# Kernel tuning notes

Hardware: AMD Instinct MI355X
Metric: run time of the kernel (lower is better)

The kernel has to match this reference:

```python
import jax, jax.numpy as jnp
import numpy as np

B, T, C, H = 16, 2048, 1024, 64

def setup_inputs() -> dict:
    key = jax.random.key(0)
    kx, kq, kk, kv = jax.random.split(key, 4)
    x = jax.random.normal(kx, (B, T, C), dtype=jnp.float32)
    Wq = jax.random.normal(kq, (C, H), dtype=jnp.float32) * (C ** -0.5)
    Wk = jax.random.normal(kk, (C, H), dtype=jnp.float32) * (C ** -0.5)
    Wv = jax.random.normal(kv, (C, H), dtype=jnp.float32) * (C ** -0.5)
    return {"x": x, "Wq": Wq, "Wk": Wk, "Wv": Wv}

def reference(x, Wq, Wk, Wv):
    # single causal self-attention head; dropout p=0.0 (identity)
    Tlen = x.shape[1]
    q = jnp.einsum('btc,ch->bth', x, Wq)  # [B,T,H]
    k = jnp.einsum('btc,ch->bth', x, Wk)
    v = jnp.einsum('btc,ch->bth', x, Wv)
    scale = q.shape[-1] ** -0.5
    scores = jnp.einsum('bth,bsh->bts', q, k) * scale  # [B,T,T]
    causal = jnp.tril(jnp.ones((Tlen, Tlen), dtype=bool))
    scores = jnp.where(causal, scores, -jnp.inf)
    weights = jax.nn.softmax(scores, axis=-1)
    out = jnp.einsum('bts,bsh->bth', weights, v)  # [B,T,H]
    return out
```

## Files before the change

### kernel.cpp

```cpp
#include <hip/hip_runtime.h>


typedef float  floatx4 __attribute__((ext_vector_type(4)));
typedef __bf16 bf16x8  __attribute__((ext_vector_type(8)));
typedef unsigned short ushort4v __attribute__((ext_vector_type(4)));
typedef unsigned int   uint2v   __attribute__((ext_vector_type(2)));
typedef unsigned int   uint4v   __attribute__((ext_vector_type(4)));

constexpr int Bn = 16;
constexpr int Tn = 2048;
constexpr int Cn = 1024;
constexpr int Hn = 64;
constexpr int BT = Bn * Tn;

constexpr float QSCALE = 0.125f * 1.44269504088896340736f;

__device__ __forceinline__ unsigned short f2b(float f) {
  unsigned int u = __builtin_bit_cast(unsigned int, f);
  u += 0x7fffu + ((u >> 16) & 1u);
  return (unsigned short)(u >> 16);
}

__device__ __forceinline__ unsigned int cvt_pk_bf16(float lo, float hi) {
  unsigned int r;
  asm("v_cvt_pk_bf16_f32 %0, %1, %2" : "=v"(r) : "v"(lo), "v"(hi));
  return r;
}

__global__ __launch_bounds__(256) void pack_w(const float* __restrict__ Wq,
                                              const float* __restrict__ Wk,
                                              const float* __restrict__ Wv,
                                              unsigned short* __restrict__ Wp) {
  int gid = blockIdx.x * 256 + threadIdx.x;
  int mat = gid >> 16;
  int rem = gid & 65535;
  int k   = rem >> 6;
  int col = rem & 63;
  const float* W = (mat == 0) ? Wq : (mat == 1) ? Wk : Wv;
  float v = W[rem];
  int kb = k >> 3, j = k & 7, ct = (mat << 2) | (col >> 4), c = col & 15;
  size_t idx = ((((size_t)ct * 128) + kb) * 16 + c) * 8 + j;
  Wp[idx] = f2b(v);
}

__global__ __launch_bounds__(256, 2) void proj_kernel(
    const float* __restrict__ x, const unsigned short* __restrict__ Wp,
    unsigned short* __restrict__ Q, unsigned short* __restrict__ K,
    unsigned short* __restrict__ Vt) {
  __shared__ alignas(16) unsigned short Bl[2][12 * 1024];

  const int tid  = threadIdx.x;
  const int wave = tid >> 6;
  const int lane = tid & 63;
  const int quad = lane >> 4;
  const int l16  = lane & 15;
  const int wr   = wave >> 1;
  const int wc   = wave & 1;
  const int rbase = blockIdx.x * 64;

  floatx4 acc[2][6];
#pragma unroll
  for (int a = 0; a < 2; ++a)
#pragma unroll
    for (int b = 0; b < 6; ++b) acc[a][b] = (floatx4){0.f, 0.f, 0.f, 0.f};

  const float* xp = x + (size_t)(rbase + wr * 32 + l16) * Cn + quad * 8;

  auto stageB = [&](int t, int buf) {
    const int kb0 = t << 3;
#pragma unroll
    for (int i = 0; i < 3; ++i) {
      const int ct = wave * 3 + i;
#pragma unroll
      for (int h = 0; h < 2; ++h) {
        const unsigned short* g =
            Wp + ((size_t)(ct * 128 + kb0 + h * 4 + quad) * 16 + l16) * 8;
        __builtin_amdgcn_global_load_lds(
            (const __attribute__((address_space(1))) void*)g,
            (__attribute__((address_space(3))) void*)&Bl[buf][ct * 1024 + h * 512],
            16, 0, 0);
      }
    }
  };

  auto loadX = [&](int t, floatx4 (&fa)[2][2][2]) {
    const int k0 = t * 64;
#pragma unroll
    for (int rg = 0; rg < 2; ++rg) {
      const float* bp = xp + rg * 16 * Cn + k0;
      fa[rg][0][0] = *reinterpret_cast<const floatx4*>(bp);
      fa[rg][0][1] = *reinterpret_cast<const floatx4*>(bp + 4);
      fa[rg][1][0] = *reinterpret_cast<const floatx4*>(bp + 32);
      fa[rg][1][1] = *reinterpret_cast<const floatx4*>(bp + 36);
    }
  };

  auto compute = [&](const floatx4 (&fa)[2][2][2], int buf) {
    bf16x8 af[2][2];
#pragma unroll
    for (int rg = 0; rg < 2; ++rg)
#pragma unroll
      for (int kk = 0; kk < 2; ++kk) {
        uint4v u;
        u[0] = cvt_pk_bf16(fa[rg][kk][0][0], fa[rg][kk][0][1]);
        u[1] = cvt_pk_bf16(fa[rg][kk][0][2], fa[rg][kk][0][3]);
        u[2] = cvt_pk_bf16(fa[rg][kk][1][0], fa[rg][kk][1][1]);
        u[3] = cvt_pk_bf16(fa[rg][kk][1][2], fa[rg][kk][1][3]);
        af[rg][kk] = __builtin_bit_cast(bf16x8, u);
      }
#pragma unroll
    for (int kk = 0; kk < 2; ++kk) {
#pragma unroll
      for (int c6 = 0; c6 < 6; ++c6) {
        const int ct = wc * 6 + c6;
        bf16x8 bfr = *reinterpret_cast<const bf16x8*>(
            &Bl[buf][ct * 1024 + (kk * 4 + quad) * 128 + l16 * 8]);
        acc[0][c6] = __builtin_amdgcn_mfma_f32_16x16x32_bf16(af[0][kk], bfr, acc[0][c6], 0, 0, 0);
        acc[1][c6] = __builtin_amdgcn_mfma_f32_16x16x32_bf16(af[1][kk], bfr, acc[1][c6], 0, 0, 0);
      }
    }
  };

  floatx4 fa0[2][2][2], fa1[2][2][2];

  stageB(0, 0);
  loadX(0, fa0);
  __syncthreads();

  for (int tt = 0; tt < 8; ++tt) {
    const int tb = tt * 2 + 1;
    stageB(tb, 1);
    loadX(tb, fa1);
    compute(fa0, 0);
    __syncthreads();
    if (tb + 1 < 16) {
      stageB(tb + 1, 0);
      loadX(tb + 1, fa0);
    }
    compute(fa1, 1);
    __syncthreads();
  }

#pragma unroll
  for (int rt = 0; rt < 2; ++rt) {
#pragma unroll
    for (int c6 = 0; c6 < 6; ++c6) {
      const int cbase  = wc * 96 + c6 * 16;
      const int rowloc = wr * 32 + rt * 16 + quad * 4;
      if (cbase < 64) {
#pragma unroll
        for (int r = 0; r < 4; ++r)
          Q[(size_t)(rbase + rowloc + r) * Hn + cbase + l16] =
              f2b(acc[rt][c6][r] * QSCALE);
      } else if (cbase < 128) {
#pragma unroll
        for (int r = 0; r < 4; ++r)
          K[(size_t)(rbase + rowloc + r) * Hn + cbase - 64 + l16] =
              f2b(acc[rt][c6][r]);
      } else {
        const int b  = rbase >> 11;
        const int t0 = (rbase & 2047) + rowloc;
        const int h  = cbase - 128 + l16;
        ushort4v v;
#pragma unroll
        for (int r = 0; r < 4; ++r) v[r] = f2b(acc[rt][c6][r]);
        *reinterpret_cast<ushort4v*>(&Vt[((size_t)b * Hn + h) * Tn + t0]) = v;
      }
    }
  }
}

__global__ __launch_bounds__(256) void flash_kernel(
    const unsigned short* __restrict__ Q, const unsigned short* __restrict__ K,
    const unsigned short* __restrict__ Vt, float* __restrict__ out) {
  __shared__ alignas(16) unsigned short P[4][16][64];
  __shared__ alignas(16) float Om[4][16][68];
  __shared__ float Ml[4][16][2];

  const int tid  = threadIdx.x;
  const int wave = tid >> 6;
  const int lane = tid & 63;
  const int quad = lane >> 4;
  const int l16  = lane & 15;

  const int b   = blockIdx.x & 15;
  const int p16 = 127 - (blockIdx.x >> 4);
  const int qbase = p16 * 16;
  const int n_tiles  = (p16 >> 2) + 1;
  const int lastTile = p16 >> 2;
  const size_t bbase  = (size_t)b * Tn * Hn;
  const size_t vtbase = (size_t)b * Hn * Tn;

  bf16x8 qf[2];
#pragma unroll
  for (int i = 0; i < 2; ++i)
    qf[i] = *reinterpret_cast<const bf16x8*>(
        &Q[bbase + (size_t)(qbase + l16) * Hn + i * 32 + quad * 8]);

  floatx4 O[4];
#pragma unroll
  for (int i = 0; i < 4; ++i) O[i] = (floatx4){0.f, 0.f, 0.f, 0.f};
  float m_r = -INFINITY, l_r = 0.f;

  const int swz  = (l16 & 7) << 3;
  const int trow = qbase + l16;

  for (int kt = wave; kt < n_tiles; kt += 4) {
    const int kvbase = kt * 64;

    bf16x8 vf[4][2];
#pragma unroll
    for (int ht = 0; ht < 4; ++ht)
#pragma unroll
      for (int kk = 0; kk < 2; ++kk)
        vf[ht][kk] = *reinterpret_cast<const bf16x8*>(
            &Vt[vtbase + (size_t)(ht * 16 + l16) * Tn + kvbase + kk * 32 + quad * 8]);

    floatx4 S[4];
    __builtin_amdgcn_s_setprio(1);
#pragma unroll
    for (int ct = 0; ct < 4; ++ct) {
      floatx4 s = (floatx4){0.f, 0.f, 0.f, 0.f};
#pragma unroll
      for (int kk = 0; kk < 2; ++kk) {
        bf16x8 kf = *reinterpret_cast<const bf16x8*>(
            &K[bbase + (size_t)(kvbase + ct * 16 + l16) * Hn + kk * 32 + quad * 8]);
        s = __builtin_amdgcn_mfma_f32_16x16x32_bf16(kf, qf[kk], s, 0, 0, 0);
      }
      S[ct] = s;
    }
    __builtin_amdgcn_s_setprio(0);

    if (kt == lastTile) {
#pragma unroll
      for (int ct = 0; ct < 4; ++ct)
#pragma unroll
        for (int r = 0; r < 4; ++r)
          if (kvbase + ct * 16 + quad * 4 + r > trow) S[ct][r] = -1e30f;
    }

    float mx0 = fmaxf(fmaxf(S[0][0], S[0][1]), fmaxf(S[0][2], S[0][3]));
    float mx1 = fmaxf(fmaxf(S[1][0], S[1][1]), fmaxf(S[1][2], S[1][3]));
    float mx2 = fmaxf(fmaxf(S[2][0], S[2][1]), fmaxf(S[2][2], S[2][3]));
    float mx3 = fmaxf(fmaxf(S[3][0], S[3][1]), fmaxf(S[3][2], S[3][3]));
    float mx  = fmaxf(fmaxf(mx0, mx1), fmaxf(mx2, mx3));
    mx = fmaxf(mx, __shfl_xor(mx, 16));
    mx = fmaxf(mx, __shfl_xor(mx, 32));
    if (mx > m_r) {
      float alpha = __builtin_amdgcn_exp2f(m_r - mx);
      l_r *= alpha;
#pragma unroll
      for (int ht = 0; ht < 4; ++ht)
#pragma unroll
        for (int r = 0; r < 4; ++r) O[ht][r] *= alpha;
      m_r = mx;
    }
    float rs = 0.f;
#pragma unroll
    for (int ct = 0; ct < 4; ++ct)
#pragma unroll
      for (int r = 0; r < 4; ++r) {
        float p = __builtin_amdgcn_exp2f(S[ct][r] - m_r);
        S[ct][r] = p;
        rs += p;
      }
    rs += __shfl_xor(rs, 16);
    rs += __shfl_xor(rs, 32);
    l_r += rs;

#pragma unroll
    for (int ct = 0; ct < 4; ++ct) {
      uint2v w;
      w[0] = cvt_pk_bf16(S[ct][0], S[ct][1]);
      w[1] = cvt_pk_bf16(S[ct][2], S[ct][3]);
      *reinterpret_cast<uint2v*>(&P[wave][l16][(ct * 16 + quad * 4) ^ swz]) = w;
    }
    bf16x8 pf0 = *reinterpret_cast<const bf16x8*>(&P[wave][l16][(quad * 8) ^ swz]);
    bf16x8 pf1 = *reinterpret_cast<const bf16x8*>(&P[wave][l16][(32 + quad * 8) ^ swz]);

    __builtin_amdgcn_s_setprio(1);
#pragma unroll
    for (int ht = 0; ht < 4; ++ht) {
      O[ht] = __builtin_amdgcn_mfma_f32_16x16x32_bf16(vf[ht][0], pf0, O[ht], 0, 0, 0);
      O[ht] = __builtin_amdgcn_mfma_f32_16x16x32_bf16(vf[ht][1], pf1, O[ht], 0, 0, 0);
    }
    __builtin_amdgcn_s_setprio(0);
  }

#pragma unroll
  for (int ht = 0; ht < 4; ++ht)
#pragma unroll
    for (int r = 0; r < 4; ++r)
      Om[wave][l16][ht * 16 + quad * 4 + r] = O[ht][r];
  if (quad == 0) {
    Ml[wave][l16][0] = m_r;
    Ml[wave][l16][1] = l_r;
  }
  __syncthreads();

  {
    const int row = tid >> 4;
    const int c4  = (tid & 15) * 4;
    float m0 = Ml[0][row][0], m1 = Ml[1][row][0];
    float m2 = Ml[2][row][0], m3 = Ml[3][row][0];
    float M = fmaxf(fmaxf(m0, m1), fmaxf(m2, m3));
    float e0 = __builtin_amdgcn_exp2f(m0 - M), e1 = __builtin_amdgcn_exp2f(m1 - M);
    float e2 = __builtin_amdgcn_exp2f(m2 - M), e3 = __builtin_amdgcn_exp2f(m3 - M);
    float L = Ml[0][row][1] * e0 + Ml[1][row][1] * e1 +
              Ml[2][row][1] * e2 + Ml[3][row][1] * e3;
    float invL = 1.0f / L;
    floatx4 o0 = *reinterpret_cast<const floatx4*>(&Om[0][row][c4]);
    floatx4 o1 = *reinterpret_cast<const floatx4*>(&Om[1][row][c4]);
    floatx4 o2 = *reinterpret_cast<const floatx4*>(&Om[2][row][c4]);
    floatx4 o3 = *reinterpret_cast<const floatx4*>(&Om[3][row][c4]);
    floatx4 res;
#pragma unroll
    for (int j = 0; j < 4; ++j)
      res[j] = (o0[j] * e0 + o1[j] * e1 + o2[j] * e2 + o3[j] * e3) * invL;
    *reinterpret_cast<floatx4*>(
        &out[bbase + (size_t)(qbase + row) * Hn + c4]) = res;
  }
}

extern "C" void kernel_launch(void* const* d_in, const int* in_sizes, int n_in,
                              void* d_out, int out_size, void* d_ws, size_t ws_size,
                              hipStream_t stream) {
  const float* x  = (const float*)d_in[0];
  const float* Wq = (const float*)d_in[1];
  const float* Wk = (const float*)d_in[2];
  const float* Wv = (const float*)d_in[3];
  float* out = (float*)d_out;

  char* ws = (char*)d_ws;
  unsigned short* Q  = (unsigned short*)(ws);
  unsigned short* Kb = (unsigned short*)(ws + ((size_t)4 << 20));
  unsigned short* Vt = (unsigned short*)(ws + ((size_t)8 << 20));
  unsigned short* Wp = (unsigned short*)(ws + ((size_t)12 << 20));

  pack_w<<<dim3(768), dim3(256), 0, stream>>>(Wq, Wk, Wv, Wp);
  proj_kernel<<<dim3(BT / 64), dim3(256), 0, stream>>>(x, Wp, Q, Kb, Vt);
  flash_kernel<<<dim3(16 * 128), dim3(256), 0, stream>>>(Q, Kb, Vt, out);
}
```

Baseline: 276.2 us.

## Process 64 query rows per flash block to reuse K/V tiles across four query subtiles

Each flash block now handles 64 query rows (four 16-row subtiles) instead of 16, so every K and V fragment loaded from memory is reused across four query subtiles. The grid shrinks from 2048 to 512 blocks and each wave keeps four sets of O accumulators and softmax stats in registers. This cuts redundant global K/V traffic. The cost is higher register pressure, fewer blocks to fill the GPU, coarser causal load balance, and a serialized epilogue that synchronizes once per subtile.

```diff
diff --git a/kernel.cpp b/kernel.cpp
--- a/kernel.cpp
+++ b/kernel.cpp
@@ -183,27 +183,32 @@
   const int quad = lane >> 4;
   const int l16  = lane & 15;
 
-  const int b   = blockIdx.x & 15;
-  const int p16 = 127 - (blockIdx.x >> 4);
-  const int qbase = p16 * 16;
-  const int n_tiles  = (p16 >> 2) + 1;
-  const int lastTile = p16 >> 2;
+  const int b  = blockIdx.x & 15;
+  const int p  = 31 - (blockIdx.x >> 4);
+  const int qbase = p * 64;
+  const int n_tiles  = p + 1;
+  const int lastTile = p;
   const size_t bbase  = (size_t)b * Tn * Hn;
   const size_t vtbase = (size_t)b * Hn * Tn;
 
-  bf16x8 qf[2];
-#pragma unroll
-  for (int i = 0; i < 2; ++i)
-    qf[i] = *reinterpret_cast<const bf16x8*>(
-        &Q[bbase + (size_t)(qbase + l16) * Hn + i * 32 + quad * 8]);
-
-  floatx4 O[4];
-#pragma unroll
-  for (int i = 0; i < 4; ++i) O[i] = (floatx4){0.f, 0.f, 0.f, 0.f};
-  float m_r = -INFINITY, l_r = 0.f;
-
-  const int swz  = (l16 & 7) << 3;
-  const int trow = qbase + l16;
+  bf16x8 qf[4][2];
+#pragma unroll
+  for (int qt = 0; qt < 4; ++qt)
+#pragma unroll
+    for (int i = 0; i < 2; ++i)
+      qf[qt][i] = *reinterpret_cast<const bf16x8*>(
+          &Q[bbase + (size_t)(qbase + qt * 16 + l16) * Hn + i * 32 + quad * 8]);
+
+  floatx4 O[4][4];
+#pragma unroll
+  for (int qt = 0; qt < 4; ++qt)
+#pragma unroll
+    for (int i = 0; i < 4; ++i) O[qt][i] = (floatx4){0.f, 0.f, 0.f, 0.f};
+  float m_r[4], l_r[4];
+#pragma unroll
+  for (int qt = 0; qt < 4; ++qt) { m_r[qt] = -INFINITY; l_r[qt] = 0.f; }
+
+  const int swz = (l16 & 7) << 3;
 
   for (int kt = wave; kt < n_tiles; kt += 4) {
     const int kvbase = kt * 64;
@@ -216,109 +221,126 @@
         vf[ht][kk] = *reinterpret_cast<const bf16x8*>(
             &Vt[vtbase + (size_t)(ht * 16 + l16) * Tn + kvbase + kk * 32 + quad * 8]);
 
-    floatx4 S[4];
-    __builtin_amdgcn_s_setprio(1);
-#pragma unroll
-    for (int ct = 0; ct < 4; ++ct) {
-      floatx4 s = (floatx4){0.f, 0.f, 0.f, 0.f};
-#pragma unroll
-      for (int kk = 0; kk < 2; ++kk) {
-        bf16x8 kf = *reinterpret_cast<const bf16x8*>(
-            &K[bbase + (size_t)(kvbase + ct * 16 + l16) * Hn + kk * 32 + quad * 8]);
-        s = __builtin_amdgcn_mfma_f32_16x16x32_bf16(kf, qf[kk], s, 0, 0, 0);
-      }
-      S[ct] = s;
-    }
-    __builtin_amdgcn_s_setprio(0);
-
-    if (kt == lastTile) {
-#pragma unroll
-      for (int ct = 0; ct < 4; ++ct)
-#pragma unroll
-        for (int r = 0; r < 4; ++r)
-          if (kvbase + ct * 16 + quad * 4 + r > trow) S[ct][r] = -1e30f;
-    }
-
-    float mx0 = fmaxf(fmaxf(S[0][0], S[0][1]), fmaxf(S[0][2], S[0][3]));
-    float mx1 = fmaxf(fmaxf(S[1][0], S[1][1]), fmaxf(S[1][2], S[1][3]));
-    float mx2 = fmaxf(fmaxf(S[2][0], S[2][1]), fmaxf(S[2][2], S[2][3]));
-    float mx3 = fmaxf(fmaxf(S[3][0], S[3][1]), fmaxf(S[3][2], S[3][3]));
-    float mx  = fmaxf(fmaxf(mx0, mx1), fmaxf(mx2, mx3));
-    mx = fmaxf(mx, __shfl_xor(mx, 16));
-    mx = fmaxf(mx, __shfl_xor(mx, 32));
-    if (mx > m_r) {
-      float alpha = __builtin_amdgcn_exp2f(m_r - mx);
-      l_r *= alpha;
-#pragma unroll
-      for (int ht = 0; ht < 4; ++ht)
-#pragma unroll
-        for (int r = 0; r < 4; ++r) O[ht][r] *= alpha;
-      m_r = mx;
-    }
-    float rs = 0.f;
-#pragma unroll
-    for (int ct = 0; ct < 4; ++ct)
-#pragma unroll
-      for (int r = 0; r < 4; ++r) {
-        float p = __builtin_amdgcn_exp2f(S[ct][r] - m_r);
-        S[ct][r] = p;
-        rs += p;
-      }
-    rs += __shfl_xor(rs, 16);
-    rs += __shfl_xor(rs, 32);
-    l_r += rs;
-
-#pragma unroll
-    for (int ct = 0; ct < 4; ++ct) {
-      uint2v w;
-      w[0] = cvt_pk_bf16(S[ct][0], S[ct][1]);
-      w[1] = cvt_pk_bf16(S[ct][2], S[ct][3]);
-      *reinterpret_cast<uint2v*>(&P[wave][l16][(ct * 16 + quad * 4) ^ swz]) = w;
-    }
-    bf16x8 pf0 = *reinterpret_cast<const bf16x8*>(&P[wave][l16][(quad * 8) ^ swz]);
-    bf16x8 pf1 = *reinterpret_cast<const bf16x8*>(&P[wave][l16][(32 + quad * 8) ^ swz]);
-
-    __builtin_amdgcn_s_setprio(1);
-#pragma unroll
-    for (int ht = 0; ht < 4; ++ht) {
-      O[ht] = __builtin_amdgcn_mfma_f32_16x16x32_bf16(vf[ht][0], pf0, O[ht], 0, 0, 0);
-      O[ht] = __builtin_amdgcn_mfma_f32_16x16x32_bf16(vf[ht][1], pf1, O[ht], 0, 0, 0);
-    }
-    __builtin_amdgcn_s_setprio(0);
+#pragma unroll
+    for (int half = 0; half < 2; ++half) {
+      floatx4 S[2][4];
+      __builtin_amdgcn_s_setprio(1);
+#pragma unroll
+      for (int ct = 0; ct < 4; ++ct) {
+        const unsigned short* kp =
+            &K[bbase + (size_t)(kvbase + ct * 16 + l16) * Hn + quad * 8];
+        bf16x8 kf0 = *reinterpret_cast<const bf16x8*>(kp);
+        bf16x8 kf1 = *reinterpret_cast<const bf16x8*>(kp + 32);
+#pragma unroll
+        for (int q2 = 0; q2 < 2; ++q2) {
+          const int qt = half * 2 + q2;
+          floatx4 s = (floatx4){0.f, 0.f, 0.f, 0.f};
+          s = __builtin_amdgcn_mfma_f32_16x16x32_bf16(kf0, qf[qt][0], s, 0, 0, 0);
+          s = __builtin_amdgcn_mfma_f32_16x16x32_bf16(kf1, qf[qt][1], s, 0, 0, 0);
+          S[q2][ct] = s;
+        }
+      }
+      __builtin_amdgcn_s_setprio(0);
+
+#pragma unroll
+      for (int q2 = 0; q2 < 2; ++q2) {
+        const int qt = half * 2 + q2;
+        const int trow = qbase + qt * 16 + l16;
+
+        if (kt == lastTile) {
+#pragma unroll
+          for (int ct = 0; ct < 4; ++ct)
+#pragma unroll
+            for (int r = 0; r < 4; ++r)
+              if (kvbase + ct * 16 + quad * 4 + r > trow) S[q2][ct][r] = -1e30f;
+        }
+
+        float mx0 = fmaxf(fmaxf(S[q2][0][0], S[q2][0][1]), fmaxf(S[q2][0][2], S[q2][0][3]));
+        float mx1 = fmaxf(fmaxf(S[q2][1][0], S[q2][1][1]), fmaxf(S[q2][1][2], S[q2][1][3]));
+        float mx2 = fmaxf(fmaxf(S[q2][2][0], S[q2][2][1]), fmaxf(S[q2][2][2], S[q2][2][3]));
+        float mx3 = fmaxf(fmaxf(S[q2][3][0], S[q2][3][1]), fmaxf(S[q2][3][2], S[q2][3][3]));
+        float mx  = fmaxf(fmaxf(mx0, mx1), fmaxf(mx2, mx3));
+        mx = fmaxf(mx, __shfl_xor(mx, 16));
+        mx = fmaxf(mx, __shfl_xor(mx, 32));
+        if (mx > m_r[qt]) {
+          float alpha = __builtin_amdgcn_exp2f(m_r[qt] - mx);
+          l_r[qt] *= alpha;
+#pragma unroll
+          for (int ht = 0; ht < 4; ++ht)
+#pragma unroll
+            for (int r = 0; r < 4; ++r) O[qt][ht][r] *= alpha;
+          m_r[qt] = mx;
+        }
+        float rs = 0.f;
+#pragma unroll
+        for (int ct = 0; ct < 4; ++ct)
+#pragma unroll
+          for (int r = 0; r < 4; ++r) {
+            float pv = __builtin_amdgcn_exp2f(S[q2][ct][r] - m_r[qt]);
+            S[q2][ct][r] = pv;
+            rs += pv;
+          }
+        rs += __shfl_xor(rs, 16);
+        rs += __shfl_xor(rs, 32);
+        l_r[qt] += rs;
+
+#pragma unroll
+        for (int ct = 0; ct < 4; ++ct) {
+          uint2v w;
+          w[0] = cvt_pk_bf16(S[q2][ct][0], S[q2][ct][1]);
+          w[1] = cvt_pk_bf16(S[q2][ct][2], S[q2][ct][3]);
+          *reinterpret_cast<uint2v*>(&P[wave][l16][(ct * 16 + quad * 4) ^ swz]) = w;
+        }
+        bf16x8 pf0 = *reinterpret_cast<const bf16x8*>(&P[wave][l16][(quad * 8) ^ swz]);
+        bf16x8 pf1 = *reinterpret_cast<const bf16x8*>(&P[wave][l16][(32 + quad * 8) ^ swz]);
+
+        __builtin_amdgcn_s_setprio(1);
+#pragma unroll
+        for (int ht = 0; ht < 4; ++ht) {
+          O[qt][ht] = __builtin_amdgcn_mfma_f32_16x16x32_bf16(vf[ht][0], pf0, O[qt][ht], 0, 0, 0);
+          O[qt][ht] = __builtin_amdgcn_mfma_f32_16x16x32_bf16(vf[ht][1], pf1, O[qt][ht], 0, 0, 0);
+        }
+        __builtin_amdgcn_s_setprio(0);
+      }
+    }
   }
 
 #pragma unroll
-  for (int ht = 0; ht < 4; ++ht)
-#pragma unroll
-    for (int r = 0; r < 4; ++r)
-      Om[wave][l16][ht * 16 + quad * 4 + r] = O[ht][r];
-  if (quad == 0) {
-    Ml[wave][l16][0] = m_r;
-    Ml[wave][l16][1] = l_r;
-  }
-  __syncthreads();
-
-  {
-    const int row = tid >> 4;
-    const int c4  = (tid & 15) * 4;
-    float m0 = Ml[0][row][0], m1 = Ml[1][row][0];
-    float m2 = Ml[2][row][0], m3 = Ml[3][row][0];
-    float M = fmaxf(fmaxf(m0, m1), fmaxf(m2, m3));
-    float e0 = __builtin_amdgcn_exp2f(m0 - M), e1 = __builtin_amdgcn_exp2f(m1 - M);
-    float e2 = __builtin_amdgcn_exp2f(m2 - M), e3 = __builtin_amdgcn_exp2f(m3 - M);
-    float L = Ml[0][row][1] * e0 + Ml[1][row][1] * e1 +
-              Ml[2][row][1] * e2 + Ml[3][row][1] * e3;
-    float invL = 1.0f / L;
-    floatx4 o0 = *reinterpret_cast<const floatx4*>(&Om[0][row][c4]);
-    floatx4 o1 = *reinterpret_cast<const floatx4*>(&Om[1][row][c4]);
-    floatx4 o2 = *reinterpret_cast<const floatx4*>(&Om[2][row][c4]);
-    floatx4 o3 = *reinterpret_cast<const floatx4*>(&Om[3][row][c4]);
-    floatx4 res;
-#pragma unroll
-    for (int j = 0; j < 4; ++j)
-      res[j] = (o0[j] * e0 + o1[j] * e1 + o2[j] * e2 + o3[j] * e3) * invL;
-    *reinterpret_cast<floatx4*>(
-        &out[bbase + (size_t)(qbase + row) * Hn + c4]) = res;
+  for (int qt = 0; qt < 4; ++qt) {
+#pragma unroll
+    for (int ht = 0; ht < 4; ++ht)
+#pragma unroll
+      for (int r = 0; r < 4; ++r)
+        Om[wave][l16][ht * 16 + quad * 4 + r] = O[qt][ht][r];
+    if (quad == 0) {
+      Ml[wave][l16][0] = m_r[qt];
+      Ml[wave][l16][1] = l_r[qt];
+    }
+    __syncthreads();
+
+    {
+      const int row = tid >> 4;
+      const int c4  = (tid & 15) * 4;
+      float m0 = Ml[0][row][0], m1 = Ml[1][row][0];
+      float m2 = Ml[2][row][0], m3 = Ml[3][row][0];
+      float M = fmaxf(fmaxf(m0, m1), fmaxf(m2, m3));
+      float e0 = __builtin_amdgcn_exp2f(m0 - M), e1 = __builtin_amdgcn_exp2f(m1 - M);
+      float e2 = __builtin_amdgcn_exp2f(m2 - M), e3 = __builtin_amdgcn_exp2f(m3 - M);
+      float L = Ml[0][row][1] * e0 + Ml[1][row][1] * e1 +
+                Ml[2][row][1] * e2 + Ml[3][row][1] * e3;
+      float invL = 1.0f / L;
+      floatx4 o0 = *reinterpret_cast<const floatx4*>(&Om[0][row][c4]);
+      floatx4 o1 = *reinterpret_cast<const floatx4*>(&Om[1][row][c4]);
+      floatx4 o2 = *reinterpret_cast<const floatx4*>(&Om[2][row][c4]);
+      floatx4 o3 = *reinterpret_cast<const floatx4*>(&Om[3][row][c4]);
+      floatx4 res;
+#pragma unroll
+      for (int j = 0; j < 4; ++j)
+        res[j] = (o0[j] * e0 + o1[j] * e1 + o2[j] * e2 + o3[j] * e3) * invL;
+      *reinterpret_cast<floatx4*>(
+          &out[bbase + (size_t)(qbase + qt * 16 + row) * Hn + c4]) = res;
+    }
+    __syncthreads();
   }
 }
 
@@ -339,5 +361,5 @@
 
   pack_w<<<dim3(768), dim3(256), 0, stream>>>(Wq, Wk, Wv, Wp);
   proj_kernel<<<dim3(BT / 64), dim3(256), 0, stream>>>(x, Wp, Q, Kb, Vt);
-  flash_kernel<<<dim3(16 * 128), dim3(256), 0, stream>>>(Q, Kb, Vt, out);
-}
+  flash_kernel<<<dim3(16 * 32), dim3(256), 0, stream>>>(Q, Kb, Vt, out);
+}
```

New measurement: 259.4 us. 6.1% less time.
